# Kernel optimization log

Hardware: AMD Instinct MI355X
Metric: run time of the kernel (lower is better)

Reference implementation:

```python
import jax, jax.numpy as jnp
import numpy as np
import math

D_SINGLE, D_PAIR, H, PQ, PV = 384, 128, 12, 4, 8
DH = D_SINGLE // H
OUT_DIM = H * DH + H * PV * 4 + H * D_PAIR


def setup_inputs() -> dict:
    key = jax.random.key(0)
    ks = jax.random.split(key, 24)
    B, L = 1, 512
    inp = {
        'single': jax.random.normal(ks[0], (B, L, D_SINGLE), jnp.float32),
        'pair': jax.random.normal(ks[1], (B, L, L, D_PAIR), jnp.float32),
        'rot_mats': jax.random.normal(ks[2], (B, L, 3, 3), jnp.float32),
        'trans': jax.random.normal(ks[3], (B, L, 3), jnp.float32),
        'mask': jnp.ones((B, L), jnp.float32),
        'ln_w': jnp.ones((D_SINGLE,), jnp.float32),
        'ln_b': jnp.zeros((D_SINGLE,), jnp.float32),
        'Wq': jax.random.normal(ks[4], (D_SINGLE, H * DH), jnp.float32) * 0.02,
        'bq': jnp.zeros((H * DH,), jnp.float32),
        'Wk': jax.random.normal(ks[5], (D_SINGLE, H * DH), jnp.float32) * 0.02,
        'bk': jnp.zeros((H * DH,), jnp.float32),
        'Wv': jax.random.normal(ks[6], (D_SINGLE, H * DH), jnp.float32) * 0.02,
        'bv': jnp.zeros((H * DH,), jnp.float32),
        'Wqp': jax.random.normal(ks[7], (D_SINGLE, H * PQ * 3), jnp.float32) * 0.02,
        'bqp': jnp.zeros((H * PQ * 3,), jnp.float32),
        'Wkp': jax.random.normal(ks[8], (D_SINGLE, H * PQ * 3), jnp.float32) * 0.02,
        'bkp': jnp.zeros((H * PQ * 3,), jnp.float32),
        'Wvp': jax.random.normal(ks[9], (D_SINGLE, H * PV * 3), jnp.float32) * 0.02,
        'bvp': jnp.zeros((H * PV * 3,), jnp.float32),
        'Wpb': jax.random.normal(ks[10], (D_PAIR, H), jnp.float32) * 0.02,
        'bpb': jnp.zeros((H,), jnp.float32),
        'Wo': jax.random.normal(ks[11], (OUT_DIM, D_SINGLE), jnp.float32) * 0.02,
        'bo': jnp.zeros((D_SINGLE,), jnp.float32),
        'w_c': jnp.asarray(1.0 / math.sqrt(3.0), jnp.float32),
        'w_l': jnp.asarray(1.0 / 3.0, jnp.float32),
        'gamma_h': jnp.ones((H,), jnp.float32),
    }
    return inp


def _layer_norm(x, w, b, eps=1e-5):
    mu = jnp.mean(x, axis=-1, keepdims=True)
    var = jnp.mean((x - mu) ** 2, axis=-1, keepdims=True)
    return (x - mu) * jax.lax.rsqrt(var + eps) * w + b


def reference(single, pair, rot_mats, trans, mask, ln_w, ln_b, Wq, bq, Wk, bk, Wv, bv,
              Wqp, bqp, Wkp, bkp, Wvp, bvp, Wpb, bpb, Wo, bo, w_c, w_l, gamma_h):
    B, L, _ = single.shape
    sn = _layer_norm(single, ln_w, ln_b)
    q = (sn @ Wq + bq).reshape(B, L, H, DH)
    k = (sn @ Wk + bk).reshape(B, L, H, DH)
    v = (sn @ Wv + bv).reshape(B, L, H, DH)
    qp = (sn @ Wqp + bqp).reshape(B, L, H, PQ, 3)
    kp = (sn @ Wkp + bkp).reshape(B, L, H, PQ, 3)
    vp = (sn @ Wvp + bvp).reshape(B, L, H, PV, 3)

    t = trans[:, :, None, None, :]  # [B,L,1,1,3]
    qg = jnp.einsum('blij,blhpj->blhpi', rot_mats, qp) + t
    kg = jnp.einsum('blij,blhpj->blhpi', rot_mats, kp) + t
    vg = jnp.einsum('blij,blhpj->blhpi', rot_mats, vp) + t

    # sequence logits [B,H,L,L]
    seq_logits = jnp.einsum('bihd,bjhd->bhij', q, k) * w_c / math.sqrt(DH)

    # geometric logits: pairwise point distances [B,H,L,L]
    q_pts = jnp.transpose(qg, (0, 2, 1, 3, 4))  # [B,H,L,PQ,3]
    k_pts = jnp.transpose(kg, (0, 2, 1, 3, 4))
    diff = q_pts[:, :, :, None] - k_pts[:, :, None]  # [B,H,L,L,PQ,3]
    dist_sq = jnp.sum(diff ** 2, axis=-1)            # [B,H,L,L,PQ]
    geo_logits = -0.5 * jnp.sum(dist_sq, axis=-1) * gamma_h[None, :, None, None] * w_l

    pair_bias = jnp.transpose(pair @ Wpb + bpb, (0, 3, 1, 2))  # [B,H,L,L]
    logits = seq_logits + geo_logits + pair_bias

    mask_2d = (mask[:, :, None] * mask[:, None, :])[:, None]  # [B,1,L,L]
    logits = jnp.where(mask_2d > 0, logits, jnp.float32(-1e9))
    attn = jax.nn.softmax(logits, axis=-1)  # [B,H,L,L]

    # sequence aggregation -> [B,L,H,DH]
    seq_out = jnp.einsum('bhij,bjhd->bihd', attn, v).reshape(B, L, H * DH)

    # point aggregation -> local frame features
    pts_out = jnp.einsum('bhij,bjhpd->bihpd', attn, vg)  # [B,L,H,PV,3]
    pts_local = jnp.einsum('blji,blhpj->blhpi', rot_mats, pts_out - t)
    pts_norm = jnp.linalg.norm(pts_local, axis=-1, keepdims=True)
    pts_feat = jnp.concatenate([pts_norm, pts_local], axis=-1).reshape(B, L, H * PV * 4)

    # pair aggregation -> [B,L,H*D_PAIR]
    pair_out = jnp.einsum('bhij,bijd->bihd', attn, pair).reshape(B, L, H * D_PAIR)

    combined = jnp.concatenate([seq_out, pts_feat, pair_out], axis=-1)
    return combined @ Wo + bo
```

## Files before the change

kernel.cpp:

```cpp
#include <hip/hip_runtime.h>
#include <math.h>

#define LQ   512
#define DS   384
#define DPAIR 128
#define NH   12
#define NP   1728
#define NPP  1792
#define FE   48

__global__ void k_concat_w(const float* __restrict__ Wq, const float* __restrict__ Wk,
                           const float* __restrict__ Wv, const float* __restrict__ Wqp,
                           const float* __restrict__ Wkp, const float* __restrict__ Wvp,
                           const float* __restrict__ bq, const float* __restrict__ bk,
                           const float* __restrict__ bv, const float* __restrict__ bqp,
                           const float* __restrict__ bkp, const float* __restrict__ bvp,
                           float* __restrict__ Wcat, float* __restrict__ bcat) {
  int idx = blockIdx.x * 256 + threadIdx.x;
  const int total = DS * NPP;
  if (idx < total) {
    int k = idx / NPP, c = idx % NPP;
    float v = 0.f;
    if (c < 384)       v = Wq[k*384 + c];
    else if (c < 768)  v = Wk[k*384 + c-384];
    else if (c < 1152) v = Wv[k*384 + c-768];
    else if (c < 1296) v = Wqp[k*144 + c-1152];
    else if (c < 1440) v = Wkp[k*144 + c-1296];
    else if (c < 1728) v = Wvp[k*288 + c-1440];
    Wcat[idx] = v;
  } else if (idx < total + NPP) {
    int c = idx - total;
    float v = 0.f;
    if (c < 384)       v = bq[c];
    else if (c < 768)  v = bk[c-384];
    else if (c < 1152) v = bv[c-768];
    else if (c < 1296) v = bqp[c-1152];
    else if (c < 1440) v = bkp[c-1296];
    else if (c < 1728) v = bvp[c-1440];
    bcat[c] = v;
  }
}

__global__ __launch_bounds__(128) void k_layernorm(const float* __restrict__ x,
                                                   const float* __restrict__ w,
                                                   const float* __restrict__ b,
                                                   float* __restrict__ y) {
  __shared__ float red[128];
  __shared__ float s_mu, s_rstd;
  int i = blockIdx.x, t = threadIdx.x;
  float v0 = x[i*DS + t], v1 = x[i*DS + t + 128], v2 = x[i*DS + t + 256];
  red[t] = v0 + v1 + v2; __syncthreads();
  for (int s = 64; s > 0; s >>= 1) { if (t < s) red[t] += red[t+s]; __syncthreads(); }
  if (t == 0) s_mu = red[0] * (1.f/384.f);
  __syncthreads();
  float mu = s_mu;
  float d0 = v0-mu, d1 = v1-mu, d2 = v2-mu;
  red[t] = d0*d0 + d1*d1 + d2*d2; __syncthreads();
  for (int s = 64; s > 0; s >>= 1) { if (t < s) red[t] += red[t+s]; __syncthreads(); }
  if (t == 0) s_rstd = rsqrtf(red[0] * (1.f/384.f) + 1e-5f);
  __syncthreads();
  float r = s_rstd;
  y[i*DS + t      ] = d0*r*w[t      ] + b[t      ];
  y[i*DS + t + 128] = d1*r*w[t + 128] + b[t + 128];
  y[i*DS + t + 256] = d2*r*w[t + 256] + b[t + 256];
}

__global__ __launch_bounds__(256) void k_gemm_nn(const float* __restrict__ A,
                                                 const float* __restrict__ B,
                                                 const float* __restrict__ bias,
                                                 float* __restrict__ C,
                                                 float* __restrict__ Cpart,
                                                 int M, int N, int K) {
  __shared__ float As[16*68];
  __shared__ float Bs[16*68];
  int t = threadIdx.x;
  int mg = t >> 4, ng = t & 15;
  int i0 = blockIdx.y * 64, j0 = blockIdx.x * 64;
  int KS = gridDim.z;
  int kper = K / KS;
  int kbeg = blockIdx.z * kper;
  float acc[4][4] = {};
  for (int k0 = kbeg; k0 < kbeg + kper; k0 += 16) {
    int e = t;
    #pragma unroll
    for (int s = 0; s < 4; s++, e += 256) {
      int m = e >> 4, k = e & 15;
      As[k*68 + m] = A[(size_t)(i0+m)*K + k0 + k];
      int k2 = e >> 6, n = e & 63;
      Bs[k2*68 + n] = B[(size_t)(k0+k2)*N + j0 + n];
    }
    __syncthreads();
    #pragma unroll
    for (int k = 0; k < 16; k++) {
      float4 av = *(const float4*)(As + k*68 + mg*4);
      float4 bv = *(const float4*)(Bs + k*68 + ng*4);
      float a[4] = {av.x, av.y, av.z, av.w};
      float b[4] = {bv.x, bv.y, bv.z, bv.w};
      #pragma unroll
      for (int y = 0; y < 4; y++)
        #pragma unroll
        for (int x = 0; x < 4; x++)
          acc[y][x] = fmaf(a[y], b[x], acc[y][x]);
    }
    __syncthreads();
  }
  if (KS == 1) {
    #pragma unroll
    for (int y = 0; y < 4; y++) {
      int m = i0 + mg*4 + y;
      #pragma unroll
      for (int x = 0; x < 4; x++) {
        int n = j0 + ng*4 + x;
        C[(size_t)m*N + n] = acc[y][x] + bias[n];
      }
    }
  } else {
    float* dst = Cpart + (size_t)blockIdx.z * M * N;
    #pragma unroll
    for (int y = 0; y < 4; y++) {
      int m = i0 + mg*4 + y;
      #pragma unroll
      for (int x = 0; x < 4; x++) {
        int n = j0 + ng*4 + x;
        dst[(size_t)m*N + n] = acc[y][x];
      }
    }
  }
}

__global__ void k_reduce_bias(const float* __restrict__ part, const float* __restrict__ bias,
                              float* __restrict__ out, int MN, int N, int KS) {
  int e = blockIdx.x * 256 + threadIdx.x;
  if (e >= MN) return;
  float s = bias[e % N];
  for (int z = 0; z < KS; z++) s += part[(size_t)z*MN + e];
  out[e] = s;
}

__global__ void k_rotate(const float* __restrict__ C1, const float* __restrict__ rot,
                         const float* __restrict__ trans, float* __restrict__ qg,
                         float* __restrict__ kg, float* __restrict__ vg) {
  int idx = blockIdx.x * 256 + threadIdx.x;
  if (idx >= LQ*NH*16) return;
  int w = idx & 15; int h = (idx >> 4) % NH; int i = idx / (16*NH);
  const float* R = rot + (size_t)i*9;
  const float* tr = trans + (size_t)i*3;
  const float* src; float* dst;
  if (w < 4)      { src = C1 + (size_t)i*NPP + 1152 + h*12 + w*3;     dst = qg + ((size_t)i*NH + h)*12 + w*3; }
  else if (w < 8) { int p = w-4; src = C1 + (size_t)i*NPP + 1296 + h*12 + p*3; dst = kg + ((size_t)i*NH + h)*12 + p*3; }
  else            { int p = w-8; src = C1 + (size_t)i*NPP + 1440 + h*24 + p*3; dst = vg + ((size_t)i*NH + h)*24 + p*3; }
  float x = src[0], y = src[1], z = src[2];
  dst[0] = fmaf(R[0],x, fmaf(R[1],y, fmaf(R[2],z, tr[0])));
  dst[1] = fmaf(R[3],x, fmaf(R[4],y, fmaf(R[5],z, tr[1])));
  dst[2] = fmaf(R[6],x, fmaf(R[7],y, fmaf(R[8],z, tr[2])));
}

__global__ void k_features(const float* __restrict__ C1, const float* __restrict__ qg,
                           const float* __restrict__ kg, const float* __restrict__ gamma,
                           const float* __restrict__ w_c, const float* __restrict__ w_l,
                           float* __restrict__ Af, float* __restrict__ Bf) {
  int idx = blockIdx.x * 256 + threadIdx.x;
  if (idx >= LQ*NH) return;
  int h = idx % NH, i = idx / NH;
  float s  = w_c[0] * rsqrtf(32.f);
  float gp = gamma[h] * w_l[0];
  float* a  = Af + ((size_t)h*LQ + i)*FE;
  float* bb = Bf + ((size_t)h*LQ + i)*FE;
  const float* q = C1 + (size_t)i*NPP + h*32;
  const float* k = C1 + (size_t)i*NPP + 384 + h*32;
  for (int d = 0; d < 32; d++) { a[d] = s*q[d]; bb[d] = k[d]; }
  const float* qp = qg + ((size_t)i*NH + h)*12;
  const float* kp = kg + ((size_t)i*NH + h)*12;
  float sq = 0.f, sk = 0.f;
  for (int d = 0; d < 12; d++) {
    float x = qp[d], y = kp[d];
    a[32+d] = gp*x; bb[32+d] = y;
    sq = fmaf(x,x,sq); sk = fmaf(y,y,sk);
  }
  a[44] = -0.5f*gp*sq; a[45] = 1.f; a[46] = 0.f; a[47] = 0.f;
  bb[44] = 1.f; bb[45] = -0.5f*gp*sk; bb[46] = 0.f; bb[47] = 0.f;
}

__global__ __launch_bounds__(256) void k_logits_nt(const float* __restrict__ Af,
                                                   const float* __restrict__ Bf,
                                                   float* __restrict__ S) {
  __shared__ float As[48*68];
  __shared__ float Bs[48*68];
  int h = blockIdx.z;
  int i0 = blockIdx.y * 64, j0 = blockIdx.x * 64;
  int t = threadIdx.x;
  int mg = t >> 4, ng = t & 15;
  const float* Ah = Af + (size_t)h*LQ*FE;
  const float* Bh = Bf + (size_t)h*LQ*FE;
  for (int e = t; e < 64*48; e += 256) {
    int m = e / 48, k = e % 48;
    As[k*68 + m] = Ah[(size_t)(i0+m)*FE + k];
    Bs[k*68 + m] = Bh[(size_t)(j0+m)*FE + k];
  }
  __syncthreads();
  float acc[4][4] = {};
  #pragma unroll 8
  for (int k = 0; k < 48; k++) {
    float4 av = *(const float4*)(As + k*68 + mg*4);
    float4 bv = *(const float4*)(Bs + k*68 + ng*4);
    float a[4] = {av.x, av.y, av.z, av.w};
    float b[4] = {bv.x, bv.y, bv.z, bv.w};
    #pragma unroll
    for (int y = 0; y < 4; y++)
      #pragma unroll
      for (int x = 0; x < 4; x++)
        acc[y][x] = fmaf(a[y], b[x], acc[y][x]);
  }
  #pragma unroll
  for (int y = 0; y < 4; y++) {
    #pragma unroll
    for (int x = 0; x < 4; x++)
      S[((size_t)h*LQ + i0 + mg*4 + y)*LQ + j0 + ng*4 + x] = acc[y][x];
  }
}

__global__ __launch_bounds__(256) void k_pair_bias(const float* __restrict__ pair,
                                                   const float* __restrict__ Wpb,
                                                   const float* __restrict__ bpb,
                                                   float* __restrict__ S) {
  int bid = blockIdx.x;
  int i = bid >> 1;
  int j = (bid & 1) * 256 + threadIdx.x;
  const float* prow = pair + ((size_t)i*LQ + j) * DPAIR;
  float acc[NH];
  #pragma unroll
  for (int h = 0; h < NH; h++) acc[h] = bpb[h];
  for (int c4 = 0; c4 < 32; c4++) {
    float4 p = *(const float4*)(prow + c4*4);
    float pv[4] = {p.x, p.y, p.z, p.w};
    #pragma unroll
    for (int cc = 0; cc < 4; cc++) {
      #pragma unroll
      for (int h = 0; h < NH; h++)
        acc[h] = fmaf(pv[cc], Wpb[(c4*4+cc)*NH + h], acc[h]);
    }
  }
  #pragma unroll
  for (int h = 0; h < NH; h++) {
    size_t idx = ((size_t)h*LQ + i)*LQ + j;
    S[idx] += acc[h];
  }
}

__global__ __launch_bounds__(512) void k_softmax(float* __restrict__ S,
                                                 const float* __restrict__ mask,
                                                 float* __restrict__ attnT) {
  __shared__ float buf[NH*LQ];
  __shared__ float red[8];
  __shared__ float bcast;
  int i = blockIdx.x, t = threadIdx.x;
  int lane = t & 63, wv = t >> 6;
  float mi = mask[i];
  float mj = mask[t];
  for (int h = 0; h < NH; h++) {
    size_t idx = ((size_t)h*LQ + i)*LQ + t;
    float l = S[idx];
    if (mi*mj <= 0.f) l = -1e9f;
    float m = l;
    for (int o = 32; o > 0; o >>= 1) m = fmaxf(m, __shfl_xor(m, o, 64));
    if (lane == 0) red[wv] = m;
    __syncthreads();
    if (t == 0) { float mm = red[0]; for (int w2 = 1; w2 < 8; w2++) mm = fmaxf(mm, red[w2]); bcast = mm; }
    __syncthreads();
    float mx = bcast;
    float e = __expf(l - mx);
    float sm = e;
    for (int o = 32; o > 0; o >>= 1) sm += __shfl_xor(sm, o, 64);
    if (lane == 0) red[wv] = sm;
    __syncthreads();
    if (t == 0) { float ss = 0.f; for (int w2 = 0; w2 < 8; w2++) ss += red[w2]; bcast = ss; }
    __syncthreads();
    float a = e / bcast;
    buf[h*LQ + t] = a;
    S[idx] = a;
    __syncthreads();
  }
  #pragma unroll
  for (int h4 = 0; h4 < 3; h4++) {
    float4 v;
    v.x = buf[(h4*4+0)*LQ + t];
    v.y = buf[(h4*4+1)*LQ + t];
    v.z = buf[(h4*4+2)*LQ + t];
    v.w = buf[(h4*4+3)*LQ + t];
    *(float4*)(attnT + ((size_t)i*LQ + t)*NH + h4*4) = v;
  }
}

__global__ __launch_bounds__(128) void k_pair_out(const float* __restrict__ attnT,
                                                  const float* __restrict__ pair,
                                                  float* __restrict__ comb) {
  __shared__ float red[NH*128];
  int i = blockIdx.x, t = threadIdx.x;
  int d2 = t & 63;
  int js = t >> 6;
  int aoff = __builtin_amdgcn_readfirstlane(js * NH);
  const float* prow = pair + (size_t)i*LQ*DPAIR + 2*d2;
  const float* arow = attnT + (size_t)i*LQ*NH + aoff;
  float acc[NH][2] = {};
  for (int jj = 0; jj < 256; jj++) {
    int j = 2*jj + js;
    float2 p = *(const float2*)(prow + (size_t)j*DPAIR);
    const float* av = arow + jj*(2*NH);
    #pragma unroll
    for (int h = 0; h < NH; h++) {
      acc[h][0] = fmaf(av[h], p.x, acc[h][0]);
      acc[h][1] = fmaf(av[h], p.y, acc[h][1]);
    }
  }
  if (js == 1) {
    #pragma unroll
    for (int h = 0; h < NH; h++) {
      red[h*128 + 2*d2    ] = acc[h][0];
      red[h*128 + 2*d2 + 1] = acc[h][1];
    }
  }
  __syncthreads();
  if (js == 0) {
    #pragma unroll
    for (int h = 0; h < NH; h++) {
      float v0 = acc[h][0] + red[h*128 + 2*d2];
      float v1 = acc[h][1] + red[h*128 + 2*d2 + 1];
      float* dst = comb + (size_t)i*2304 + 768 + h*128 + 2*d2;
      dst[0] = v0; dst[1] = v1;
    }
  }
}

__global__ __launch_bounds__(256) void k_attn_v(const float* __restrict__ attn,
                                                const float* __restrict__ C1,
                                                const float* __restrict__ vg,
                                                float* __restrict__ psum) {
  __shared__ float As[64*68];
  __shared__ float Vs[64*68];
  int i0 = blockIdx.x * 64;
  int h = blockIdx.y;
  int z = blockIdx.z;
  int t = threadIdx.x;
  int mg = t >> 4, ng = t & 15;
  float acc[4][4] = {};
  for (int k0 = z*128; k0 < z*128 + 128; k0 += 64) {
    __syncthreads();
    for (int e = t; e < 64*64; e += 256) {
      int m = e >> 6, j = e & 63;
      As[j*68 + m] = attn[((size_t)h*LQ + i0 + m)*LQ + k0 + j];
    }
    for (int e = t; e < 64*64; e += 256) {
      int j = e >> 6, c = e & 63;
      float v = 0.f;
      if (c < 32)      v = C1[(size_t)(k0+j)*NPP + 768 + h*32 + c];
      else if (c < 56) v = vg[((size_t)(k0+j)*NH + h)*24 + (c-32)];
      Vs[j*68 + c] = v;
    }
    __syncthreads();
    #pragma unroll 4
    for (int j = 0; j < 64; j++) {
      float4 av = *(const float4*)(As + j*68 + mg*4);
      float4 bv = *(const float4*)(Vs + j*68 + ng*4);
      float a[4] = {av.x, av.y, av.z, av.w};
      float b[4] = {bv.x, bv.y, bv.z, bv.w};
      #pragma unroll
      for (int y = 0; y < 4; y++)
        #pragma unroll
        for (int x = 0; x < 4; x++)
          acc[y][x] = fmaf(a[y], b[x], acc[y][x]);
    }
  }
  #pragma unroll
  for (int y = 0; y < 4; y++) {
    int i = i0 + mg*4 + y;
    #pragma unroll
    for (int x = 0; x < 4; x++) {
      int n = ng*4 + x;
      psum[(((size_t)z*LQ + i)*NH + h)*64 + n] = acc[y][x];
    }
  }
}

__global__ void k_av_reduce(const float* __restrict__ psum, float* __restrict__ comb,
                            float* __restrict__ pts) {
  int e = blockIdx.x * 256 + threadIdx.x;
  if (e >= LQ*NH*56) return;
  int n = e % 56; int ih = e / 56; int h = ih % NH; int i = ih / NH;
  size_t base = ((size_t)i*NH + h)*64 + n;
  float s = 0.f;
  for (int z = 0; z < 4; z++) s += psum[(size_t)z*LQ*NH*64 + base];
  if (n < 32) comb[(size_t)i*2304 + h*32 + n] = s;
  else        pts[((size_t)i*NH + h)*24 + (n-32)] = s;
}

__global__ void k_pts_feat(const float* __restrict__ pts, const float* __restrict__ rot,
                           const float* __restrict__ trans, float* __restrict__ comb) {
  int idx = blockIdx.x * 256 + threadIdx.x;
  if (idx >= LQ*NH*8) return;
  int p = idx & 7; int h = (idx >> 3) % NH; int i = idx / (8*NH);
  const float* R = rot + (size_t)i*9;
  const float* tr = trans + (size_t)i*3;
  const float* pt = pts + ((size_t)i*NH + h)*24 + p*3;
  float x = pt[0]-tr[0], y = pt[1]-tr[1], z = pt[2]-tr[2];
  float lx = fmaf(R[0],x, fmaf(R[3],y, R[6]*z));
  float ly = fmaf(R[1],x, fmaf(R[4],y, R[7]*z));
  float lz = fmaf(R[2],x, fmaf(R[5],y, R[8]*z));
  float nrm = sqrtf(fmaf(lx,lx, fmaf(ly,ly, lz*lz)));
  float* dst = comb + (size_t)i*2304 + 384 + (h*8 + p)*4;
  dst[0] = nrm; dst[1] = lx; dst[2] = ly; dst[3] = lz;
}

extern "C" void kernel_launch(void* const* d_in, const int* in_sizes, int n_in,
                              void* d_out, int out_size, void* d_ws, size_t ws_size,
                              hipStream_t stream) {
  const float* single = (const float*)d_in[0];
  const float* pair   = (const float*)d_in[1];
  const float* rot    = (const float*)d_in[2];
  const float* trans  = (const float*)d_in[3];
  const float* mask   = (const float*)d_in[4];
  const float* ln_w   = (const float*)d_in[5];
  const float* ln_b   = (const float*)d_in[6];
  const float* Wq     = (const float*)d_in[7];
  const float* bq     = (const float*)d_in[8];
  const float* Wk     = (const float*)d_in[9];
  const float* bk     = (const float*)d_in[10];
  const float* Wv     = (const float*)d_in[11];
  const float* bv     = (const float*)d_in[12];
  const float* Wqp    = (const float*)d_in[13];
  const float* bqp    = (const float*)d_in[14];
  const float* Wkp    = (const float*)d_in[15];
  const float* bkp    = (const float*)d_in[16];
  const float* Wvp    = (const float*)d_in[17];
  const float* bvp    = (const float*)d_in[18];
  const float* Wpb    = (const float*)d_in[19];
  const float* bpb    = (const float*)d_in[20];
  const float* Wo     = (const float*)d_in[21];
  const float* bo     = (const float*)d_in[22];
  const float* w_c    = (const float*)d_in[23];
  const float* w_l    = (const float*)d_in[24];
  const float* gamma  = (const float*)d_in[25];
  float* out = (float*)d_out;

  float* p = (float*)d_ws;
  auto alloc = [&](size_t n) { float* r = p; p += n; return r; };
  float* Wcat   = alloc((size_t)DS*NPP);
  float* bcat   = alloc(NPP);
  float* sn     = alloc((size_t)LQ*DS);
  float* C1     = alloc((size_t)LQ*NPP);
  float* qg     = alloc((size_t)LQ*NH*12);
  float* kg     = alloc((size_t)LQ*NH*12);
  float* vgb    = alloc((size_t)LQ*NH*24);
  float* Af     = alloc((size_t)NH*LQ*FE);
  float* Bf     = alloc((size_t)NH*LQ*FE);
  float* S      = alloc((size_t)NH*LQ*LQ);
  float* attnT  = alloc((size_t)LQ*LQ*NH);
  float* comb   = alloc((size_t)LQ*2304);
  float* pts    = alloc((size_t)LQ*NH*24);
  float* scratch= alloc((size_t)8*LQ*DS);

  k_concat_w<<<dim3((DS*NPP + NPP + 255)/256), 256, 0, stream>>>(
      Wq, Wk, Wv, Wqp, Wkp, Wvp, bq, bk, bv, bqp, bkp, bvp, Wcat, bcat);
  k_layernorm<<<dim3(LQ), 128, 0, stream>>>(single, ln_w, ln_b, sn);
  k_gemm_nn<<<dim3(NPP/64, LQ/64, 1), 256, 0, stream>>>(sn, Wcat, bcat, C1, nullptr, LQ, NPP, DS);
  k_rotate<<<dim3((LQ*NH*16 + 255)/256), 256, 0, stream>>>(C1, rot, trans, qg, kg, vgb);
  k_features<<<dim3((LQ*NH + 255)/256), 256, 0, stream>>>(C1, qg, kg, gamma, w_c, w_l, Af, Bf);
  k_logits_nt<<<dim3(LQ/64, LQ/64, NH), 256, 0, stream>>>(Af, Bf, S);
  k_pair_bias<<<dim3(LQ*2), 256, 0, stream>>>(pair, Wpb, bpb, S);
  k_softmax<<<dim3(LQ), 512, 0, stream>>>(S, mask, attnT);
  k_pair_out<<<dim3(LQ), 128, 0, stream>>>(attnT, pair, comb);
  k_attn_v<<<dim3(LQ/64, NH, 4), 256, 0, stream>>>(S, C1, vgb, scratch);
  k_av_reduce<<<dim3((LQ*NH*56 + 255)/256), 256, 0, stream>>>(scratch, comb, pts);
  k_pts_feat<<<dim3((LQ*NH*8 + 255)/256), 256, 0, stream>>>(pts, rot, trans, comb);
  k_gemm_nn<<<dim3(DS/64, LQ/64, 8), 256, 0, stream>>>(comb, Wo, bo, nullptr, scratch, LQ, DS, 2304);
  k_reduce_bias<<<dim3((LQ*DS + 255)/256), 256, 0, stream>>>(scratch, bo, out, LQ*DS, DS, 8);
}
```

Baseline: 431.1 us.

## Fuse pair bias, softmax and pair aggregation into one online-softmax kernel

Replaces the separate pair-bias, softmax and pair-output kernels with a single per-row kernel. It streams each pair row tile through shared memory once, computes the bias projection, runs an online softmax across tiles and accumulates the attention-weighted pair sum. This removes the second full read of the large pair tensor and the attnT intermediate buffer. A small kernel transposes Wpb for vectorized weight reads. Large shared memory use and register pressure may limit occupancy.

```diff
diff --git a/kernel.cpp b/kernel.cpp
--- a/kernel.cpp
+++ b/kernel.cpp
@@ -5,9 +5,9 @@
 #define DS   384
 #define DPAIR 128
 #define NH   12
-#define NP   1728
 #define NPP  1792
 #define FE   48
+#define TJ   128
 
 __global__ void k_concat_w(const float* __restrict__ Wq, const float* __restrict__ Wk,
                            const float* __restrict__ Wv, const float* __restrict__ Wqp,
@@ -41,6 +41,13 @@
   }
 }
 
+__global__ void k_wpbt(const float* __restrict__ Wpb, float* __restrict__ WpbT) {
+  int e = blockIdx.x * 256 + threadIdx.x;
+  if (e >= DPAIR * NH) return;
+  int k = e / NH, h = e % NH;
+  WpbT[h*DPAIR + k] = Wpb[e];
+}
+
 __global__ __launch_bounds__(128) void k_layernorm(const float* __restrict__ x,
                                                    const float* __restrict__ w,
                                                    const float* __restrict__ b,
@@ -219,115 +226,167 @@
   }
 }
 
-__global__ __launch_bounds__(256) void k_pair_bias(const float* __restrict__ pair,
-                                                   const float* __restrict__ Wpb,
-                                                   const float* __restrict__ bpb,
-                                                   float* __restrict__ S) {
-  int bid = blockIdx.x;
-  int i = bid >> 1;
-  int j = (bid & 1) * 256 + threadIdx.x;
-  const float* prow = pair + ((size_t)i*LQ + j) * DPAIR;
-  float acc[NH];
+__global__ __launch_bounds__(512, 2) void k_pair_fused(
+    const float* __restrict__ pair, const float* __restrict__ WpbT,
+    const float* __restrict__ bpb, const float* __restrict__ mask,
+    float* __restrict__ S, float* __restrict__ comb) {
+  __shared__ float tile[TJ*133];
+  __shared__ float logit[NH*LQ];
+  __shared__ float wt[NH*TJ];
+  __shared__ float m_s[NH], s_s[NH], alpha_s[NH];
+  int i = blockIdx.x, t = threadIdx.x;
+  float mi = mask[i];
+
+  for (int e = t; e < NH*LQ; e += 512) {
+    int h = e >> 9, j = e & 511;
+    logit[e] = S[((size_t)h*LQ + i)*LQ + j] + bpb[h];
+  }
+  if (t < NH) { m_s[t] = -3.0e38f; s_s[t] = 0.f; alpha_s[t] = 0.f; }
+
+  const float* psrc = pair + (size_t)i*LQ*DPAIR;
+  float4 r[8];
   #pragma unroll
-  for (int h = 0; h < NH; h++) acc[h] = bpb[h];
-  for (int c4 = 0; c4 < 32; c4++) {
-    float4 p = *(const float4*)(prow + c4*4);
-    float pv[4] = {p.x, p.y, p.z, p.w};
-    #pragma unroll
-    for (int cc = 0; cc < 4; cc++) {
-      #pragma unroll
-      for (int h = 0; h < NH; h++)
-        acc[h] = fmaf(pv[cc], Wpb[(c4*4+cc)*NH + h], acc[h]);
-    }
-  }
+  for (int u = 0; u < 8; u++) r[u] = ((const float4*)psrc)[t + u*512];
+
+  float4 acc[NH];
   #pragma unroll
-  for (int h = 0; h < NH; h++) {
-    size_t idx = ((size_t)h*LQ + i)*LQ + j;
-    S[idx] += acc[h];
-  }
-}
-
-__global__ __launch_bounds__(512) void k_softmax(float* __restrict__ S,
-                                                 const float* __restrict__ mask,
-                                                 float* __restrict__ attnT) {
-  __shared__ float buf[NH*LQ];
-  __shared__ float red[8];
-  __shared__ float bcast;
-  int i = blockIdx.x, t = threadIdx.x;
-  int lane = t & 63, wv = t >> 6;
-  float mi = mask[i];
-  float mj = mask[t];
-  for (int h = 0; h < NH; h++) {
-    size_t idx = ((size_t)h*LQ + i)*LQ + t;
-    float l = S[idx];
-    if (mi*mj <= 0.f) l = -1e9f;
-    float m = l;
-    for (int o = 32; o > 0; o >>= 1) m = fmaxf(m, __shfl_xor(m, o, 64));
-    if (lane == 0) red[wv] = m;
-    __syncthreads();
-    if (t == 0) { float mm = red[0]; for (int w2 = 1; w2 < 8; w2++) mm = fmaxf(mm, red[w2]); bcast = mm; }
-    __syncthreads();
-    float mx = bcast;
-    float e = __expf(l - mx);
-    float sm = e;
-    for (int o = 32; o > 0; o >>= 1) sm += __shfl_xor(sm, o, 64);
-    if (lane == 0) red[wv] = sm;
-    __syncthreads();
-    if (t == 0) { float ss = 0.f; for (int w2 = 0; w2 < 8; w2++) ss += red[w2]; bcast = ss; }
-    __syncthreads();
-    float a = e / bcast;
-    buf[h*LQ + t] = a;
-    S[idx] = a;
-    __syncthreads();
-  }
+  for (int h = 0; h < NH; h++) acc[h] = make_float4(0.f,0.f,0.f,0.f);
+
+  for (int jt = 0; jt < LQ/TJ; jt++) {
+    #pragma unroll
+    for (int u = 0; u < 8; u++) {
+      int e = t + u*512; int row = e >> 5, c4 = e & 31;
+      *(float4*)&tile[row*133 + c4*4] = r[u];
+    }
+    __syncthreads();
+    if (jt < LQ/TJ - 1) {
+      const float4* nsrc = (const float4*)(psrc + (size_t)(jt+1)*TJ*DPAIR);
+      #pragma unroll
+      for (int u = 0; u < 8; u++) r[u] = nsrc[t + u*512];
+    }
+
+    {
+      int j = t & 127;
+      int hg = __builtin_amdgcn_readfirstlane(t >> 7);
+      const float* w0p = WpbT + (hg*3+0)*DPAIR;
+      const float* w1p = WpbT + (hg*3+1)*DPAIR;
+      const float* w2p = WpbT + (hg*3+2)*DPAIR;
+      float a0 = 0.f, a1 = 0.f, a2 = 0.f;
+      #pragma unroll 8
+      for (int k = 0; k < DPAIR; k += 4) {
+        float4 pv = *(const float4*)&tile[j*133 + k];
+        float4 w0 = *(const float4*)(w0p + k);
+        float4 w1 = *(const float4*)(w1p + k);
+        float4 w2 = *(const float4*)(w2p + k);
+        a0 = fmaf(pv.x,w0.x, fmaf(pv.y,w0.y, fmaf(pv.z,w0.z, fmaf(pv.w,w0.w, a0))));
+        a1 = fmaf(pv.x,w1.x, fmaf(pv.y,w1.y, fmaf(pv.z,w1.z, fmaf(pv.w,w1.w, a1))));
+        a2 = fmaf(pv.x,w2.x, fmaf(pv.y,w2.y, fmaf(pv.z,w2.z, fmaf(pv.w,w2.w, a2))));
+      }
+      int jj = jt*TJ + j;
+      bool dead = (mi * mask[jj] <= 0.f);
+      int h0 = hg*3;
+      float l0 = logit[(h0+0)*LQ + jj] + a0;
+      float l1 = logit[(h0+1)*LQ + jj] + a1;
+      float l2 = logit[(h0+2)*LQ + jj] + a2;
+      if (dead) { l0 = -1e9f; l1 = -1e9f; l2 = -1e9f; }
+      logit[(h0+0)*LQ + jj] = l0;
+      logit[(h0+1)*LQ + jj] = l1;
+      logit[(h0+2)*LQ + jj] = l2;
+    }
+    __syncthreads();
+
+    float lv[4];
+    int sh = t >> 5, sl = t & 31;
+    if (t < NH*32) {
+      float mx = -3.0e38f;
+      #pragma unroll
+      for (int q = 0; q < 4; q++) {
+        lv[q] = logit[sh*LQ + jt*TJ + sl + q*32];
+        mx = fmaxf(mx, lv[q]);
+      }
+      #pragma unroll
+      for (int o = 16; o > 0; o >>= 1) mx = fmaxf(mx, __shfl_xor(mx, o));
+      if (sl == 0) {
+        float mo = m_s[sh];
+        float mn = fmaxf(mo, mx);
+        alpha_s[sh] = __expf(mo - mn);
+        m_s[sh] = mn;
+      }
+    }
+    __syncthreads();
+    if (t < NH*32) {
+      float mn = m_s[sh];
+      float sm = 0.f;
+      #pragma unroll
+      for (int q = 0; q < 4; q++) {
+        float w = __expf(lv[q] - mn);
+        wt[sh*TJ + sl + q*32] = w;
+        sm += w;
+      }
+      #pragma unroll
+      for (int o = 16; o > 0; o >>= 1) sm += __shfl_xor(sm, o);
+      if (sl == 0) s_s[sh] = s_s[sh]*alpha_s[sh] + sm;
+    }
+    __syncthreads();
+
+    {
+      int dg = t & 31, strip = t >> 5;
+      int jb = strip*8;
+      float4 pv[8];
+      #pragma unroll
+      for (int q = 0; q < 8; q++) pv[q] = *(const float4*)&tile[(jb+q)*133 + dg*4];
+      #pragma unroll
+      for (int h = 0; h < NH; h++) {
+        float al = alpha_s[h];
+        float4 w0 = *(const float4*)&wt[h*TJ + jb];
+        float4 w1 = *(const float4*)&wt[h*TJ + jb + 4];
+        float wq[8] = {w0.x,w0.y,w0.z,w0.w,w1.x,w1.y,w1.z,w1.w};
+        float4 a = acc[h];
+        a.x *= al; a.y *= al; a.z *= al; a.w *= al;
+        #pragma unroll
+        for (int q = 0; q < 8; q++) {
+          a.x = fmaf(wq[q], pv[q].x, a.x);
+          a.y = fmaf(wq[q], pv[q].y, a.y);
+          a.z = fmaf(wq[q], pv[q].z, a.z);
+          a.w = fmaf(wq[q], pv[q].w, a.w);
+        }
+        acc[h] = a;
+      }
+    }
+    __syncthreads();
+  }
+
+  for (int e = t; e < NH*LQ; e += 512) {
+    int h = e >> 9, j = e & 511;
+    float a = __expf(logit[e] - m_s[h]) / s_s[h];
+    S[((size_t)h*LQ + i)*LQ + j] = a;
+  }
+
+  float4* red4 = (float4*)tile;
+  int dg = t & 31, strip = t >> 5;
+  float4 tot = make_float4(0.f,0.f,0.f,0.f);
   #pragma unroll
-  for (int h4 = 0; h4 < 3; h4++) {
-    float4 v;
-    v.x = buf[(h4*4+0)*LQ + t];
-    v.y = buf[(h4*4+1)*LQ + t];
-    v.z = buf[(h4*4+2)*LQ + t];
-    v.w = buf[(h4*4+3)*LQ + t];
-    *(float4*)(attnT + ((size_t)i*LQ + t)*NH + h4*4) = v;
-  }
-}
-
-__global__ __launch_bounds__(128) void k_pair_out(const float* __restrict__ attnT,
-                                                  const float* __restrict__ pair,
-                                                  float* __restrict__ comb) {
-  __shared__ float red[NH*128];
-  int i = blockIdx.x, t = threadIdx.x;
-  int d2 = t & 63;
-  int js = t >> 6;
-  int aoff = __builtin_amdgcn_readfirstlane(js * NH);
-  const float* prow = pair + (size_t)i*LQ*DPAIR + 2*d2;
-  const float* arow = attnT + (size_t)i*LQ*NH + aoff;
-  float acc[NH][2] = {};
-  for (int jj = 0; jj < 256; jj++) {
-    int j = 2*jj + js;
-    float2 p = *(const float2*)(prow + (size_t)j*DPAIR);
-    const float* av = arow + jj*(2*NH);
-    #pragma unroll
-    for (int h = 0; h < NH; h++) {
-      acc[h][0] = fmaf(av[h], p.x, acc[h][0]);
-      acc[h][1] = fmaf(av[h], p.y, acc[h][1]);
-    }
-  }
-  if (js == 1) {
-    #pragma unroll
-    for (int h = 0; h < NH; h++) {
-      red[h*128 + 2*d2    ] = acc[h][0];
-      red[h*128 + 2*d2 + 1] = acc[h][1];
-    }
-  }
-  __syncthreads();
-  if (js == 0) {
-    #pragma unroll
-    for (int h = 0; h < NH; h++) {
-      float v0 = acc[h][0] + red[h*128 + 2*d2];
-      float v1 = acc[h][1] + red[h*128 + 2*d2 + 1];
-      float* dst = comb + (size_t)i*2304 + 768 + h*128 + 2*d2;
-      dst[0] = v0; dst[1] = v1;
-    }
+  for (int half = 0; half < 2; half++) {
+    if ((strip >> 3) == half) {
+      #pragma unroll
+      for (int h = 0; h < NH; h++) red4[((strip & 7)*NH + h)*32 + dg] = acc[h];
+    }
+    __syncthreads();
+    if (t < NH*32) {
+      int h = t >> 5, d = t & 31;
+      #pragma unroll
+      for (int s8 = 0; s8 < 8; s8++) {
+        float4 v = red4[(s8*NH + h)*32 + d];
+        tot.x += v.x; tot.y += v.y; tot.z += v.z; tot.w += v.w;
+      }
+    }
+    __syncthreads();
+  }
+  if (t < NH*32) {
+    int h = t >> 5, d = t & 31;
+    float is = 1.f / s_s[h];
+    float4 o = make_float4(tot.x*is, tot.y*is, tot.z*is, tot.w*is);
+    *(float4*)&comb[(size_t)i*2304 + 768 + h*DPAIR + d*4] = o;
   }
 }
 
@@ -445,6 +504,7 @@
   auto alloc = [&](size_t n) { float* r = p; p += n; return r; };
   float* Wcat   = alloc((size_t)DS*NPP);
   float* bcat   = alloc(NPP);
+  float* WpbT   = alloc((size_t)NH*DPAIR);
   float* sn     = alloc((size_t)LQ*DS);
   float* C1     = alloc((size_t)LQ*NPP);
   float* qg     = alloc((size_t)LQ*NH*12);
@@ -453,21 +513,19 @@
   float* Af     = alloc((size_t)NH*LQ*FE);
   float* Bf     = alloc((size_t)NH*LQ*FE);
   float* S      = alloc((size_t)NH*LQ*LQ);
-  float* attnT  = alloc((size_t)LQ*LQ*NH);
   float* comb   = alloc((size_t)LQ*2304);
   float* pts    = alloc((size_t)LQ*NH*24);
   float* scratch= alloc((size_t)8*LQ*DS);
 
   k_concat_w<<<dim3((DS*NPP + NPP + 255)/256), 256, 0, stream>>>(
       Wq, Wk, Wv, Wqp, Wkp, Wvp, bq, bk, bv, bqp, bkp, bvp, Wcat, bcat);
+  k_wpbt<<<dim3((DPAIR*NH + 255)/256), 256, 0, stream>>>(Wpb, WpbT);
   k_layernorm<<<dim3(LQ), 128, 0, stream>>>(single, ln_w, ln_b, sn);
   k_gemm_nn<<<dim3(NPP/64, LQ/64, 1), 256, 0, stream>>>(sn, Wcat, bcat, C1, nullptr, LQ, NPP, DS);
   k_rotate<<<dim3((LQ*NH*16 + 255)/256), 256, 0, stream>>>(C1, rot, trans, qg, kg, vgb);
   k_features<<<dim3((LQ*NH + 255)/256), 256, 0, stream>>>(C1, qg, kg, gamma, w_c, w_l, Af, Bf);
   k_logits_nt<<<dim3(LQ/64, LQ/64, NH), 256, 0, stream>>>(Af, Bf, S);
-  k_pair_bias<<<dim3(LQ*2), 256, 0, stream>>>(pair, Wpb, bpb, S);
-  k_softmax<<<dim3(LQ), 512, 0, stream>>>(S, mask, attnT);
-  k_pair_out<<<dim3(LQ), 128, 0, stream>>>(attnT, pair, comb);
+  k_pair_fused<<<dim3(LQ), 512, 0, stream>>>(pair, WpbT, bpb, mask, S, comb);
   k_attn_v<<<dim3(LQ/64, NH, 4), 256, 0, stream>>>(S, C1, vgb, scratch);
   k_av_reduce<<<dim3((LQ*NH*56 + 255)/256), 256, 0, stream>>>(scratch, comb, pts);
   k_pts_feat<<<dim3((LQ*NH*8 + 255)/256), 256, 0, stream>>>(pts, rot, trans, comb);
```

Result: faster. 418.0 us (-3.0%).
